# Kernel tuning notes

Measured on AMD Instinct MI355X. Metric: run time of the kernel, lower is better.

Reference implementation:

```python
import jax, jax.numpy as jnp
import numpy as np

B, N, DIM = 4, 16384, 256
H, D, G = 8, 64, 32  # heads, dim_head, slice_num; inner = H*D = 512


def setup_inputs() -> dict:
    key = jax.random.key(0)
    ks = jax.random.split(key, 12)
    inner = H * D
    s = lambda fan_in: 1.0 / np.sqrt(fan_in)
    inp = {
        "x": jax.random.normal(ks[0], (B, N, DIM), jnp.float32),
        # weights stored (in, out) so forward is x @ W + b
        "Wfx": jax.random.uniform(ks[1], (DIM, inner), jnp.float32, -s(DIM), s(DIM)),
        "bfx": jnp.zeros((inner,), jnp.float32),
        "Wx": jax.random.uniform(ks[2], (DIM, inner), jnp.float32, -s(DIM), s(DIM)),
        "bx": jnp.zeros((inner,), jnp.float32),
        "Wslice": jnp.linalg.qr(jax.random.normal(ks[3], (D, G), jnp.float32))[0],  # orthogonal init
        "bslice": jnp.zeros((G,), jnp.float32),
        "temperature": jnp.full((1, H, 1, 1), 0.5, jnp.float32),
        "Wq": jax.random.uniform(ks[4], (D, D), jnp.float32, -s(D), s(D)),
        "Wk": jax.random.uniform(ks[5], (D, D), jnp.float32, -s(D), s(D)),
        "Wv": jax.random.uniform(ks[6], (D, D), jnp.float32, -s(D), s(D)),
        "Wout": jax.random.uniform(ks[7], (inner, DIM), jnp.float32, -s(inner), s(inner)),
        "bout": jnp.zeros((DIM,), jnp.float32),
    }
    return inp


def reference(x, Wfx, bfx, Wx, bx, Wslice, bslice, temperature, Wq, Wk, Wv, Wout, bout):
    b, n, _ = x.shape
    # projections -> [B, H, N, D]
    fx_mid = (x @ Wfx + bfx).reshape(b, n, H, D).transpose(0, 2, 1, 3)
    x_mid = (x @ Wx + bx).reshape(b, n, H, D).transpose(0, 2, 1, 3)
    # soft slice assignment: [B, H, N, G]
    slice_logits = (x_mid @ Wslice + bslice) / temperature
    slice_weights = jax.nn.softmax(slice_logits, axis=-1)
    slice_norm = slice_weights.sum(axis=2)  # [B, H, G]
    # soft pooling to G slice tokens: [B, H, G, D]
    slice_token = jnp.einsum("bhnd,bhng->bhgd", fx_mid, slice_weights)
    slice_token = slice_token / (slice_norm[..., None] + 1e-5)
    # tiny attention over G tokens
    q = slice_token @ Wq
    k = slice_token @ Wk
    v = slice_token @ Wv
    scores = jnp.einsum("bhgd,bhkd->bhgk", q, k) / jnp.sqrt(jnp.asarray(D, q.dtype))
    attn = jax.nn.softmax(scores, axis=-1)
    out_slice = jnp.einsum("bhgk,bhkd->bhgd", attn, v)
    # scatter back to N points: [B, H, N, D] -> [B, N, H*D]
    out_x = jnp.einsum("bhgd,bhng->bhnd", out_slice, slice_weights)
    out_x = out_x.transpose(0, 2, 1, 3).reshape(b, n, H * D)
    return out_x @ Wout + bout
```

## Files before the change

kernel.cpp:

```cpp
#include <hip/hip_runtime.h>


typedef unsigned short u16;
typedef __attribute__((ext_vector_type(8))) unsigned short ushort8v;
typedef __attribute__((ext_vector_type(4))) unsigned short ushort4v;
typedef __attribute__((ext_vector_type(8))) short short8v;
typedef __attribute__((ext_vector_type(4))) float f32x4;

constexpr int Nc = 16384;
constexpr int BNc = 65536;

__device__ inline float b2f(u16 v) {
    union { unsigned int u; float f; } t; t.u = ((unsigned int)v) << 16; return t.f;
}
__device__ inline u16 f2b(float f) {
    union { float f; unsigned int u; } t; t.f = f;
    unsigned int u = t.u;
    return (u16)((u + 0x7fffu + ((u >> 16) & 1u)) >> 16);
}

__global__ __launch_bounds__(256) void k0_fold(
    const float* __restrict__ Wx, const float* __restrict__ Wslice,
    const float* __restrict__ bx, const float* __restrict__ bslice,
    u16* __restrict__ WxsT, float* __restrict__ bxs)
{
    int blk = blockIdx.x, tid = threadIdx.x;
    int h = tid >> 5, g = tid & 31;
    if (blk < 256) {
        int k = blk;
        float acc = 0.f;
        for (int d = 0; d < 64; d++)
            acc += Wx[k * 512 + h * 64 + d] * Wslice[d * 32 + g];
        WxsT[tid * 256 + k] = f2b(acc);
    } else {
        float acc = 0.f;
        for (int d = 0; d < 64; d++)
            acc += bx[h * 64 + d] * Wslice[d * 32 + g];
        bxs[tid] = acc + bslice[g];
    }
}

__global__ __launch_bounds__(256) void kprep_wfx(const float* __restrict__ Wfx,
                                                 u16* __restrict__ WfxT)
{
    int n = blockIdx.x, k = threadIdx.x;
    WfxT[n * 256 + k] = f2b(Wfx[k * 512 + n]);
}

template <int MODE>
__global__ __launch_bounds__(256) void kgemm(
    const void* __restrict__ Ap, const u16* __restrict__ Bt,
    const float* __restrict__ bias, const float* __restrict__ temp,
    void* __restrict__ O1, u16* __restrict__ O2, int Kd)
{
    __shared__ u16 Asl[4][64][8];
    __shared__ u16 Bsl[4][64][8];
    int tid = threadIdx.x;
    int wave = tid >> 6, lane = tid & 63;
    int lm = lane & 15, quad = lane >> 4;
    int row0 = blockIdx.y * 64, col0 = blockIdx.x * 64;
    int sm = tid >> 2, skb = tid & 3;
    const u16* BtB = Bt;
    if (MODE == 2) BtB += (size_t)(row0 >> 14) * 65536;
    f32x4 acc[4] = {};

    for (int k0 = 0; k0 < Kd; k0 += 32) {
        if (MODE < 2) {
            const float* A32 = (const float*)Ap;
            const f32x4* src = (const f32x4*)(A32 + (size_t)(row0 + sm) * Kd + k0 + skb * 8);
            f32x4 v0 = src[0], v1 = src[1];
            ushort8v o;
#pragma unroll
            for (int j = 0; j < 4; j++) { o[j] = f2b(v0[j]); o[4 + j] = f2b(v1[j]); }
            *(ushort8v*)&Asl[skb][sm][0] = o;
        } else {
            const u16* A16 = (const u16*)Ap;
            *(ushort8v*)&Asl[skb][sm][0] =
                *(const ushort8v*)(A16 + (size_t)(row0 + sm) * Kd + k0 + skb * 8);
        }
        *(ushort8v*)&Bsl[skb][sm][0] =
            *(const ushort8v*)(BtB + (size_t)(col0 + sm) * Kd + k0 + skb * 8);
        __syncthreads();
        short8v af = *(short8v*)&Asl[quad][wave * 16 + lm][0];
#pragma unroll
        for (int nt = 0; nt < 4; nt++) {
            short8v bf = *(short8v*)&Bsl[quad][nt * 16 + lm][0];
            acc[nt] = __builtin_amdgcn_mfma_f32_16x16x32_bf16(af, bf, acc[nt], 0, 0, 0);
        }
        __syncthreads();
    }

    if (MODE == 0) {
        u16* fxT = (u16*)O1;
        int nbase = row0 + wave * 16 + quad * 4;
#pragma unroll
        for (int nt = 0; nt < 4; nt++) {
            int c = col0 + nt * 16 + lm;
            float bv = bias[c];
            ushort4v o;
#pragma unroll
            for (int r = 0; r < 4; r++) o[r] = f2b(acc[nt][r] + bv);
            *(ushort4v*)(fxT + (size_t)c * 65536 + nbase) = o;
        }
    } else if (MODE == 1) {
        int b = row0 >> 14, h0 = col0 >> 5;
        int nlbase = (row0 & 16383) + wave * 16 + quad * 4;
        u16* swb = (u16*)O1;
        float it0 = 1.0f / temp[h0], it1 = 1.0f / temp[h0 + 1];
#pragma unroll
        for (int hh = 0; hh < 2; hh++) {
            float it = hh ? it1 : it0;
            float bv0 = bias[col0 + hh * 32 + lm];
            float bv1 = bias[col0 + hh * 32 + 16 + lm];
            ushort4v p0, p1;
#pragma unroll
            for (int r = 0; r < 4; r++) {
                float v0 = (acc[2 * hh][r] + bv0) * it;
                float v1 = (acc[2 * hh + 1][r] + bv1) * it;
                float m = fmaxf(v0, v1);
                m = fmaxf(m, __shfl_xor(m, 1));
                m = fmaxf(m, __shfl_xor(m, 2));
                m = fmaxf(m, __shfl_xor(m, 4));
                m = fmaxf(m, __shfl_xor(m, 8));
                float e0 = __expf(v0 - m), e1 = __expf(v1 - m);
                float s = e0 + e1;
                s += __shfl_xor(s, 1);
                s += __shfl_xor(s, 2);
                s += __shfl_xor(s, 4);
                s += __shfl_xor(s, 8);
                float rs = 1.0f / s;
                float w0 = e0 * rs, w1 = e1 * rs;
                int row = row0 + wave * 16 + quad * 4 + r;
                swb[(size_t)row * 256 + col0 + hh * 32 + lm] = f2b(w0);
                swb[(size_t)row * 256 + col0 + hh * 32 + 16 + lm] = f2b(w1);
                p0[r] = f2b(w0); p1[r] = f2b(w1);
            }
            size_t gbase = (size_t)((b * 8 + h0 + hh) * 32);
            *(ushort4v*)(O2 + (gbase + lm) * 16384 + nlbase) = p0;
            *(ushort4v*)(O2 + (gbase + 16 + lm) * 16384 + nlbase) = p1;
        }
    } else {
        float* out = (float*)O1;
#pragma unroll
        for (int nt = 0; nt < 4; nt++) {
            int c = col0 + nt * 16 + lm;
            float bv = bias[c];
#pragma unroll
            for (int r = 0; r < 4; r++)
                out[(size_t)(row0 + wave * 16 + quad * 4 + r) * 256 + c] = acc[nt][r] + bv;
        }
    }
}

__global__ __launch_bounds__(256) void k4_token_mfma(
    const u16* __restrict__ swT, const u16* __restrict__ fxT,
    float* __restrict__ token_part, float* __restrict__ norm_part)
{
    int bh = blockIdx.x, ky = blockIdx.y;
    int b = bh >> 3, h = bh & 7;
    int tid = threadIdx.x, wave = tid >> 6, lane = tid & 63;
    int lm = lane & 15, quad = lane >> 4;
    int mt = wave & 1, dp = wave >> 1;
    const u16* Ar = swT + ((size_t)(bh * 32 + mt * 16 + lm)) * 16384 + ky * 512 + quad * 8;
    const u16* Br0 = fxT + ((size_t)(h * 64 + dp * 32 + lm)) * 65536
                     + (size_t)b * 16384 + ky * 512 + quad * 8;
    const u16* Br1 = Br0 + (size_t)16 * 65536;
    f32x4 acc0 = {}, acc1 = {};
    float nacc = 0.f;
#pragma unroll
    for (int kk = 0; kk < 16; kk++) {
        short8v af = *(const short8v*)(Ar + kk * 32);
        short8v b0 = *(const short8v*)(Br0 + kk * 32);
        short8v b1 = *(const short8v*)(Br1 + kk * 32);
        acc0 = __builtin_amdgcn_mfma_f32_16x16x32_bf16(af, b0, acc0, 0, 0, 0);
        acc1 = __builtin_amdgcn_mfma_f32_16x16x32_bf16(af, b1, acc1, 0, 0, 0);
        if (dp == 0) {
            ushort8v au = (ushort8v&)af;
#pragma unroll
            for (int j = 0; j < 8; j++) nacc += b2f(au[j]);
        }
    }
    float* tp = token_part + ((size_t)(ky * 32 + bh)) * 2048;
#pragma unroll
    for (int r = 0; r < 4; r++) {
        int g = mt * 16 + quad * 4 + r;
        tp[g * 64 + dp * 32 + lm] = acc0[r];
        tp[g * 64 + dp * 32 + 16 + lm] = acc1[r];
    }
    if (dp == 0) {
        nacc += __shfl_xor(nacc, 16);
        nacc += __shfl_xor(nacc, 32);
        if (lane < 16)
            norm_part[(ky * 32 + bh) * 32 + mt * 16 + lm] = nacc;
    }
}

__global__ __launch_bounds__(256) void k4b_reduce(
    const float* __restrict__ tp, const float* __restrict__ np,
    float* __restrict__ tl)
{
    int t = blockIdx.x * 256 + threadIdx.x;
    int bh = t >> 11, e = t & 2047, g = e >> 6;
    float ts = 0.f, ns = 0.f;
    for (int ch = 0; ch < 32; ch++) {
        ts += tp[((size_t)(ch * 32 + bh)) * 2048 + e];
        ns += np[(ch * 32 + bh) * 32 + g];
    }
    tl[t] = ts / (ns + 1e-5f);
}

__global__ __launch_bounds__(256) void k5_attn(
    const float* __restrict__ tlg,
    const float* __restrict__ Wq, const float* __restrict__ Wk, const float* __restrict__ Wv,
    float* __restrict__ out_slice)
{
    __shared__ float tl[32][64];
    __shared__ float ql[32][64], kl[32][64], vl[32][64];
    __shared__ float sl[32][33];
    int bh = blockIdx.x, tid = threadIdx.x;
    const float* tk = tlg + (size_t)bh * 2048;

#pragma unroll
    for (int j = 0; j < 8; j++) {
        int idx = j * 256 + tid;
        tl[idx >> 6][idx & 63] = tk[idx];
    }
    __syncthreads();
#pragma unroll
    for (int j = 0; j < 8; j++) {
        int idx = j * 256 + tid;
        int g = idx >> 6, d = idx & 63;
        float aq = 0.f, ak = 0.f, av = 0.f;
        for (int e = 0; e < 64; e++) {
            float t = tl[g][e];
            aq += t * Wq[e * 64 + d];
            ak += t * Wk[e * 64 + d];
            av += t * Wv[e * 64 + d];
        }
        ql[g][d] = aq; kl[g][d] = ak; vl[g][d] = av;
    }
    __syncthreads();
#pragma unroll
    for (int j = 0; j < 4; j++) {
        int idx = j * 256 + tid;
        int gq = idx >> 5, gk = idx & 31;
        float s = 0.f;
        for (int d = 0; d < 64; d++) s += ql[gq][d] * kl[gk][d];
        sl[gq][gk] = s * 0.125f;
    }
    __syncthreads();
    if (tid < 32) {
        float m = -1e30f;
        for (int k2 = 0; k2 < 32; k2++) m = fmaxf(m, sl[tid][k2]);
        float s = 0.f;
        for (int k2 = 0; k2 < 32; k2++) { float e = __expf(sl[tid][k2] - m); sl[tid][k2] = e; s += e; }
        float r = 1.0f / s;
        for (int k2 = 0; k2 < 32; k2++) sl[tid][k2] *= r;
    }
    __syncthreads();
#pragma unroll
    for (int j = 0; j < 8; j++) {
        int idx = j * 256 + tid;
        int g = idx >> 6, d = idx & 63;
        float a = 0.f;
        for (int k2 = 0; k2 < 32; k2++) a += sl[g][k2] * vl[k2][d];
        out_slice[(size_t)bh * 2048 + idx] = a;
    }
}

__global__ __launch_bounds__(256) void kZ(
    const float* __restrict__ os, const float* __restrict__ Wout,
    u16* __restrict__ ZT)
{
    int b = blockIdx.x, cb = blockIdx.y;
    int t = threadIdx.x;
    int c = cb * 16 + (t & 15), kq = t >> 4;
    for (int k = kq * 16; k < kq * 16 + 16; k++) {
        int h = k >> 5, g = k & 31;
        const float* osr = os + ((size_t)(b * 8 + h)) * 2048 + g * 64;
        float acc = 0.f;
        for (int d = 0; d < 64; d++)
            acc += osr[d] * Wout[(h * 64 + d) * 256 + c];
        ZT[(size_t)b * 65536 + c * 256 + k] = f2b(acc);
    }
}

extern "C" void kernel_launch(void* const* d_in, const int* in_sizes, int n_in,
                              void* d_out, int out_size, void* d_ws, size_t ws_size,
                              hipStream_t stream)
{
    const float* x      = (const float*)d_in[0];
    const float* Wfx    = (const float*)d_in[1];
    const float* bfx    = (const float*)d_in[2];
    const float* Wx     = (const float*)d_in[3];
    const float* bx     = (const float*)d_in[4];
    const float* Wslice = (const float*)d_in[5];
    const float* bslice = (const float*)d_in[6];
    const float* temp   = (const float*)d_in[7];
    const float* Wq     = (const float*)d_in[8];
    const float* Wk     = (const float*)d_in[9];
    const float* Wv     = (const float*)d_in[10];
    const float* Wout   = (const float*)d_in[11];
    const float* bout   = (const float*)d_in[12];

    char* ws = (char*)d_ws;
    size_t off = 0;
    auto alloc = [&](size_t bytes) {
        void* p = ws + off;
        off = (off + bytes + 255) & ~(size_t)255;
        return p;
    };
    u16*   fxT   = (u16*)  alloc((size_t)512 * BNc * 2);
    u16*   swb   = (u16*)  alloc((size_t)BNc * 256 * 2);
    u16*   swT   = (u16*)  alloc((size_t)1024 * Nc * 2);
    float* tp    = (float*)alloc((size_t)1024 * 2048 * 4);
    float* np    = (float*)alloc(32768 * 4);
    float* tl    = (float*)alloc(65536 * 4);
    float* osl   = (float*)alloc(65536 * 4);
    u16*   ZT    = (u16*)  alloc(4 * 65536 * 2);
    u16*   WfxT  = (u16*)  alloc(512 * 256 * 2);
    u16*   WxsT  = (u16*)  alloc(256 * 256 * 2);
    float* bxs   = (float*)alloc(256 * 4);

    k0_fold<<<257, 256, 0, stream>>>(Wx, Wslice, bx, bslice, WxsT, bxs);
    kprep_wfx<<<512, 256, 0, stream>>>(Wfx, WfxT);

    kgemm<0><<<dim3(8, 1024), 256, 0, stream>>>(x, WfxT, bfx, nullptr, fxT, nullptr, 256);

    kgemm<1><<<dim3(4, 1024), 256, 0, stream>>>(x, WxsT, bxs, temp, swb, swT, 256);

    k4_token_mfma<<<dim3(32, 32), 256, 0, stream>>>(swT, fxT, tp, np);
    k4b_reduce<<<256, 256, 0, stream>>>(tp, np, tl);
    k5_attn<<<32, 256, 0, stream>>>(tl, Wq, Wk, Wv, osl);
    kZ<<<dim3(4, 16), 256, 0, stream>>>(osl, Wout, ZT);

    kgemm<2><<<dim3(4, 1024), 256, 0, stream>>>(swb, ZT, bout, nullptr, d_out, nullptr, 256);
}
```

Baseline: 400.2 us.

## Make each GEMM block cover the full output width to reuse the converted A tile

The GEMM kernel is templated on the number of 16-column tiles, so each block now computes all output columns (512 for fx, 256 for slice logits and output) for its 64 rows, instead of a 64-column slice. The fp32 x rows are loaded and converted to bf16 once per row block instead of once per column block, which cuts redundant global reads and conversions. In the slice mode all 8 heads' softmax runs in one block. The cost is more accumulator registers per thread (up to 32 f32x4), a larger B tile staged per k-step, and fewer blocks (1024). Occupancy may drop or registers may spill despite the launch-bounds hint.

```diff
diff --git a/kernel.cpp b/kernel.cpp
--- a/kernel.cpp
+++ b/kernel.cpp
@@ -47,22 +47,23 @@
     WfxT[n * 256 + k] = f2b(Wfx[k * 512 + n]);
 }
 
-template <int MODE>
-__global__ __launch_bounds__(256) void kgemm(
+template <int MODE, int NT>
+__global__ __launch_bounds__(256, 2) void kgemm(
     const void* __restrict__ Ap, const u16* __restrict__ Bt,
     const float* __restrict__ bias, const float* __restrict__ temp,
-    void* __restrict__ O1, u16* __restrict__ O2, int Kd)
-{
+    void* __restrict__ O1, u16* __restrict__ O2)
+{
+    constexpr int Kd = 256;
     __shared__ u16 Asl[4][64][8];
-    __shared__ u16 Bsl[4][64][8];
+    __shared__ u16 Bsl[NT * 16][4][8];
     int tid = threadIdx.x;
     int wave = tid >> 6, lane = tid & 63;
     int lm = lane & 15, quad = lane >> 4;
-    int row0 = blockIdx.y * 64, col0 = blockIdx.x * 64;
+    int row0 = blockIdx.x * 64;
     int sm = tid >> 2, skb = tid & 3;
     const u16* BtB = Bt;
     if (MODE == 2) BtB += (size_t)(row0 >> 14) * 65536;
-    f32x4 acc[4] = {};
+    f32x4 acc[NT] = {};
 
     for (int k0 = 0; k0 < Kd; k0 += 32) {
         if (MODE < 2) {
@@ -78,13 +79,18 @@
             *(ushort8v*)&Asl[skb][sm][0] =
                 *(const ushort8v*)(A16 + (size_t)(row0 + sm) * Kd + k0 + skb * 8);
         }
-        *(ushort8v*)&Bsl[skb][sm][0] =
-            *(const ushort8v*)(BtB + (size_t)(col0 + sm) * Kd + k0 + skb * 8);
+#pragma unroll
+        for (int i = 0; i < NT / 4; i++) {
+            int e = i * 256 + tid;
+            int sn = e >> 2, sk = e & 3;
+            *(ushort8v*)&Bsl[sn][sk][0] =
+                *(const ushort8v*)(BtB + (size_t)sn * Kd + k0 + sk * 8);
+        }
         __syncthreads();
         short8v af = *(short8v*)&Asl[quad][wave * 16 + lm][0];
 #pragma unroll
-        for (int nt = 0; nt < 4; nt++) {
-            short8v bf = *(short8v*)&Bsl[quad][nt * 16 + lm][0];
+        for (int nt = 0; nt < NT; nt++) {
+            short8v bf = *(short8v*)&Bsl[nt * 16 + lm][quad][0];
             acc[nt] = __builtin_amdgcn_mfma_f32_16x16x32_bf16(af, bf, acc[nt], 0, 0, 0);
         }
         __syncthreads();
@@ -94,8 +100,8 @@
         u16* fxT = (u16*)O1;
         int nbase = row0 + wave * 16 + quad * 4;
 #pragma unroll
-        for (int nt = 0; nt < 4; nt++) {
-            int c = col0 + nt * 16 + lm;
+        for (int nt = 0; nt < NT; nt++) {
+            int c = nt * 16 + lm;
             float bv = bias[c];
             ushort4v o;
 #pragma unroll
@@ -103,20 +109,19 @@
             *(ushort4v*)(fxT + (size_t)c * 65536 + nbase) = o;
         }
     } else if (MODE == 1) {
-        int b = row0 >> 14, h0 = col0 >> 5;
+        int b = row0 >> 14;
         int nlbase = (row0 & 16383) + wave * 16 + quad * 4;
         u16* swb = (u16*)O1;
-        float it0 = 1.0f / temp[h0], it1 = 1.0f / temp[h0 + 1];
-#pragma unroll
-        for (int hh = 0; hh < 2; hh++) {
-            float it = hh ? it1 : it0;
-            float bv0 = bias[col0 + hh * 32 + lm];
-            float bv1 = bias[col0 + hh * 32 + 16 + lm];
+#pragma unroll
+        for (int h = 0; h < 8; h++) {
+            float it = 1.0f / temp[h];
+            float bv0 = bias[h * 32 + lm];
+            float bv1 = bias[h * 32 + 16 + lm];
             ushort4v p0, p1;
 #pragma unroll
             for (int r = 0; r < 4; r++) {
-                float v0 = (acc[2 * hh][r] + bv0) * it;
-                float v1 = (acc[2 * hh + 1][r] + bv1) * it;
+                float v0 = (acc[2 * h][r] + bv0) * it;
+                float v1 = (acc[2 * h + 1][r] + bv1) * it;
                 float m = fmaxf(v0, v1);
                 m = fmaxf(m, __shfl_xor(m, 1));
                 m = fmaxf(m, __shfl_xor(m, 2));
@@ -131,19 +136,19 @@
                 float rs = 1.0f / s;
                 float w0 = e0 * rs, w1 = e1 * rs;
                 int row = row0 + wave * 16 + quad * 4 + r;
-                swb[(size_t)row * 256 + col0 + hh * 32 + lm] = f2b(w0);
-                swb[(size_t)row * 256 + col0 + hh * 32 + 16 + lm] = f2b(w1);
+                swb[(size_t)row * 256 + h * 32 + lm] = f2b(w0);
+                swb[(size_t)row * 256 + h * 32 + 16 + lm] = f2b(w1);
                 p0[r] = f2b(w0); p1[r] = f2b(w1);
             }
-            size_t gbase = (size_t)((b * 8 + h0 + hh) * 32);
+            size_t gbase = (size_t)((b * 8 + h) * 32);
             *(ushort4v*)(O2 + (gbase + lm) * 16384 + nlbase) = p0;
             *(ushort4v*)(O2 + (gbase + 16 + lm) * 16384 + nlbase) = p1;
         }
     } else {
         float* out = (float*)O1;
 #pragma unroll
-        for (int nt = 0; nt < 4; nt++) {
-            int c = col0 + nt * 16 + lm;
+        for (int nt = 0; nt < NT; nt++) {
+            int c = nt * 16 + lm;
             float bv = bias[c];
 #pragma unroll
             for (int r = 0; r < 4; r++)
@@ -325,14 +330,14 @@
     k0_fold<<<257, 256, 0, stream>>>(Wx, Wslice, bx, bslice, WxsT, bxs);
     kprep_wfx<<<512, 256, 0, stream>>>(Wfx, WfxT);
 
-    kgemm<0><<<dim3(8, 1024), 256, 0, stream>>>(x, WfxT, bfx, nullptr, fxT, nullptr, 256);
-
-    kgemm<1><<<dim3(4, 1024), 256, 0, stream>>>(x, WxsT, bxs, temp, swb, swT, 256);
+    kgemm<0, 32><<<1024, 256, 0, stream>>>(x, WfxT, bfx, nullptr, fxT, nullptr);
+
+    kgemm<1, 16><<<1024, 256, 0, stream>>>(x, WxsT, bxs, temp, swb, swT);
 
     k4_token_mfma<<<dim3(32, 32), 256, 0, stream>>>(swT, fxT, tp, np);
     k4b_reduce<<<256, 256, 0, stream>>>(tp, np, tl);
     k5_attn<<<32, 256, 0, stream>>>(tl, Wq, Wk, Wv, osl);
     kZ<<<dim3(4, 16), 256, 0, stream>>>(osl, Wout, ZT);
 
-    kgemm<2><<<dim3(4, 1024), 256, 0, stream>>>(swb, ZT, bout, nullptr, d_out, nullptr, 256);
-}
+    kgemm<2, 16><<<1024, 256, 0, stream>>>(swb, ZT, bout, nullptr, d_out, nullptr);
+}
```

Measured after the change: 383.3 us. 4.2% less time.
